# Performance work log

Hardware: AMD Instinct MI355X
Metric: run time of the kernel (lower is better)

Reference implementation:

```python
import jax, jax.numpy as jnp
import numpy as np

NEG_INF = -1e30  # stand-in for -inf in additive causal mask (softmax-safe)


def rotary_pos_emb(x):
    # x: [B, T, H, D]. Faithful to source: freqs = 1/1000**(arange(0,D,2)//D)
    # with INTEGER floor division -> exponent 0 -> all freqs == 1.0.
    B, T, H, D = x.shape
    exponents = (jnp.arange(0, D, 2)[: D // 2] // D).astype(jnp.float32)
    freqs = 1.0 / jnp.power(jnp.float32(1000.0), exponents)          # [D/2]
    theta = jnp.arange(T, dtype=jnp.float32)[:, None] * freqs[None, :]  # [T, D/2]
    cos = jnp.cos(theta)[None, :, None, :]  # [1, T, 1, D/2]
    sin = jnp.sin(theta)[None, :, None, :]
    xr = x.astype(jnp.float32).reshape(B, T, H, D // 2, 2)
    x0, x1 = xr[..., 0], xr[..., 1]
    # complex multiply (x0 + i x1) * (cos + i sin)
    out = jnp.stack([x0 * cos - x1 * sin, x0 * sin + x1 * cos], axis=-1)
    return out.reshape(B, T, H, D).astype(x.dtype)


def attention_fwd(x, wq, wk, wv, wo, n_heads=32):
    B, T, C = x.shape
    hd = C // n_heads  # head_dim = 128
    # nn.Linear(bias=False): y = x @ W^T with W: [out, in]
    xq = (x @ wq.T).reshape(B, T, n_heads, hd)
    xk = (x @ wk.T).reshape(B, T, n_heads, hd)
    xv = (x @ wv.T).reshape(B, T, n_heads, hd)
    xq = rotary_pos_emb(xq)
    xk = rotary_pos_emb(xk)
    # n_rep == 1 -> repeat_kv is identity
    scale = hd ** -0.5
    scores = jnp.einsum('bqhd,bkhd->bhqk', xq, xk) * scale  # [B,H,T,T]
    causal = jnp.tril(jnp.ones((T, T), dtype=bool))
    scores = jnp.where(causal[None, None], scores, NEG_INF)
    probs = jax.nn.softmax(scores.astype(jnp.float32), axis=-1).astype(xq.dtype)
    out = jnp.einsum('bhqk,bkhd->bqhd', probs, xv).reshape(B, T, C)
    return out @ wo.T


def setup_inputs() -> dict:
    key = jax.random.key(0)
    ks = jax.random.split(key, 5)
    B, T, C = 2, 2048, 4096
    s = 0.02
    return {
        'x': jax.random.normal(ks[0], (B, T, C), jnp.float32),
        'wq': jax.random.normal(ks[1], (C, C), jnp.float32) * s,
        'wk': jax.random.normal(ks[2], (C, C), jnp.float32) * s,
        'wv': jax.random.normal(ks[3], (C, C), jnp.float32) * s,
        'wo': jax.random.normal(ks[4], (C, C), jnp.float32) * s,
    }


def reference(x, wq, wk, wv, wo):
    return attention_fwd(x, wq, wk, wv, wo)
```

## Files before the change

### kernel.cpp

```cpp
#include <hip/hip_runtime.h>
#include <hip/hip_bf16.h>
#include <stdint.h>

typedef __bf16 bf16_t;
typedef __attribute__((ext_vector_type(8))) __bf16 bf16x8;
typedef __attribute__((ext_vector_type(4))) float f32x4;

#define GLL16(gptr, lptr)                                                      \
  __builtin_amdgcn_global_load_lds(                                            \
      (__attribute__((address_space(1))) void*)(gptr),                         \
      (__attribute__((address_space(3))) void*)(lptr), 16, 0, 0)

__global__ __launch_bounds__(256) void cast5_kernel(const float* __restrict__ x,
                                                    const float* __restrict__ wq,
                                                    const float* __restrict__ wk,
                                                    const float* __restrict__ wv,
                                                    const float* __restrict__ wo,
                                                    bf16_t* __restrict__ outbase) {
  const size_t SZ = (size_t)4096 * 4096;
  const float* in;
  switch (blockIdx.y) {
    case 0: in = x; break;
    case 1: in = wq; break;
    case 2: in = wk; break;
    case 3: in = wv; break;
    default: in = wo; break;
  }
  bf16_t* out = outbase + (size_t)blockIdx.y * SZ;
  int i = blockIdx.x * 256 + threadIdx.x;
  const float4* p = (const float4*)in + (size_t)i * 2;
  float4 a = p[0], b = p[1];
  bf16x8 o;
  o[0] = (__bf16)a.x; o[1] = (__bf16)a.y; o[2] = (__bf16)a.z; o[3] = (__bf16)a.w;
  o[4] = (__bf16)b.x; o[5] = (__bf16)b.y; o[6] = (__bf16)b.z; o[7] = (__bf16)b.w;
  *((bf16x8*)out + i) = o;
}

__device__ __forceinline__ void epi_rope(f32x4 acc[4][4], bf16_t* C, int bm,
                                         int bn, int wr, int wc, int quad,
                                         int l15) {
#pragma unroll
  for (int mi = 0; mi < 4; ++mi) {
    const int row0 = bm + wr * 64 + mi * 16 + quad * 4;
    float fsv[4], fcv[4];
#pragma unroll
    for (int r = 0; r < 4; ++r)
      sincosf((float)((row0 + r) & 2047), &fsv[r], &fcv[r]);
#pragma unroll
    for (int ni = 0; ni < 4; ++ni) {
      const int col = bn + wc * 64 + ni * 16 + l15;
      const bool odd = (col & 1);
#pragma unroll
      for (int r = 0; r < 4; ++r) {
        float v = acc[mi][ni][r];
        float p = __shfl_xor(v, 1, 64);
        float o = odd ? (p * fsv[r] + v * fcv[r]) : (v * fcv[r] - p * fsv[r]);
        C[(size_t)(row0 + r) * 4096 + col] = (__bf16)o;
      }
    }
  }
}

__device__ __forceinline__ void epi_vt(f32x4 acc[4][4], bf16_t* VT, int bm,
                                       int bn, int wr, int wc, int quad,
                                       int l15) {
#pragma unroll
  for (int mi = 0; mi < 4; ++mi) {
    const int row0 = bm + wr * 64 + mi * 16 + quad * 4;
    const int b = row0 >> 11, t0 = row0 & 2047;
#pragma unroll
    for (int ni = 0; ni < 4; ++ni) {
      const int col = bn + wc * 64 + ni * 16 + l15;
      const int h = col >> 7, d = col & 127;
      union { __bf16 e[4]; uint2 u; } pk;
#pragma unroll
      for (int r = 0; r < 4; ++r) pk.e[r] = (__bf16)acc[mi][ni][r];
      *(uint2*)&VT[((size_t)((b * 32 + h) * 128 + d)) * 2048 + t0] = pk.u;
    }
  }
}

#define GEMM_MAIN_LOOP(Aptr, Bptr)                                             \
  const int c0 = w * 2, c1 = c0 + 1;                                           \
  const int ra = lane >> 2;                                                    \
  const int gsw = ((lane & 3) ^ (ra & 3)) * 8;                                 \
  const bf16_t* ga0 = Aptr + (size_t)(bm + c0 * 16 + ra) * 4096 + gsw;         \
  const bf16_t* ga1 = Aptr + (size_t)(bm + c1 * 16 + ra) * 4096 + gsw;         \
  const bf16_t* gb0 = Bptr + (size_t)(bn + c0 * 16 + ra) * 4096 + gsw;         \
  const bf16_t* gb1 = Bptr + (size_t)(bn + c1 * 16 + ra) * 4096 + gsw;         \
  f32x4 acc[4][4] = {};                                                        \
  GLL16(ga0, &As[0][c0 * 512]);                                                \
  GLL16(ga1, &As[0][c1 * 512]);                                                \
  GLL16(gb0, &Bs[0][c0 * 512]);                                                \
  GLL16(gb1, &Bs[0][c1 * 512]);                                                \
  const int sa = quad ^ (l15 & 3);                      \
  for (int kt = 0; kt < 128; ++kt) {                                           \
    const int p = kt & 1;                                                      \
    __syncthreads();     \
    if (kt != 127) {                                                           \
      const int k1 = (kt + 1) * 32;                                            \
      GLL16(ga0 + k1, &As[p ^ 1][c0 * 512]);                                   \
      GLL16(ga1 + k1, &As[p ^ 1][c1 * 512]);                                   \
      GLL16(gb0 + k1, &Bs[p ^ 1][c0 * 512]);                                   \
      GLL16(gb1 + k1, &Bs[p ^ 1][c1 * 512]);                                   \
    }                                                                          \
    bf16x8 af[4], bfr[4];                                                      \
    _Pragma("unroll") for (int mi = 0; mi < 4; ++mi)                           \
        af[mi] = *(const bf16x8*)&As[p][(wr * 64 + mi * 16 + l15) * 32 + sa * 8]; \
    _Pragma("unroll") for (int ni = 0; ni < 4; ++ni)                           \
        bfr[ni] = *(const bf16x8*)&Bs[p][(wc * 64 + ni * 16 + l15) * 32 + sa * 8]; \
    _Pragma("unroll") for (int mi = 0; mi < 4; ++mi)                           \
        _Pragma("unroll") for (int ni = 0; ni < 4; ++ni)                       \
            acc[mi][ni] = __builtin_amdgcn_mfma_f32_16x16x32_bf16(              \
                af[mi], bfr[ni], acc[mi][ni], 0, 0, 0);                        \
  }

__global__ __launch_bounds__(256) void gemm_qkv(const bf16_t* __restrict__ X,
                                                const bf16_t* __restrict__ WQ,
                                                const bf16_t* __restrict__ WK,
                                                const bf16_t* __restrict__ WV,
                                                bf16_t* __restrict__ Qo,
                                                bf16_t* __restrict__ Ko,
                                                bf16_t* __restrict__ VTo) {
  __shared__ bf16_t As[2][128 * 32];
  __shared__ bf16_t Bs[2][128 * 32];
  const int tid = threadIdx.x;
  const int w = tid >> 6;
  const int lane = tid & 63;
  const int quad = lane >> 4;
  const int l15 = lane & 15;
  const int wr = w >> 1, wc = w & 1;
  const int mat = blockIdx.x >> 5;
  const int bn = (blockIdx.x & 31) * 128, bm = blockIdx.y * 128;
  const bf16_t* Bp = (mat == 0) ? WQ : (mat == 1) ? WK : WV;

  GEMM_MAIN_LOOP(X, Bp)

  if (mat == 0)
    epi_rope(acc, Qo, bm, bn, wr, wc, quad, l15);
  else if (mat == 1)
    epi_rope(acc, Ko, bm, bn, wr, wc, quad, l15);
  else
    epi_vt(acc, VTo, bm, bn, wr, wc, quad, l15);
}

__global__ __launch_bounds__(256) void gemm_out(const bf16_t* __restrict__ A,
                                                const bf16_t* __restrict__ B,
                                                float* __restrict__ C) {
  __shared__ bf16_t As[2][128 * 32];
  __shared__ bf16_t Bs[2][128 * 32];
  const int tid = threadIdx.x;
  const int w = tid >> 6;
  const int lane = tid & 63;
  const int quad = lane >> 4;
  const int l15 = lane & 15;
  const int wr = w >> 1, wc = w & 1;
  const int bn = blockIdx.x * 128, bm = blockIdx.y * 128;

  GEMM_MAIN_LOOP(A, B)

#pragma unroll
  for (int mi = 0; mi < 4; ++mi) {
    const int row0 = bm + wr * 64 + mi * 16 + quad * 4;
#pragma unroll
    for (int ni = 0; ni < 4; ++ni) {
      const int col = bn + wc * 64 + ni * 16 + l15;
#pragma unroll
      for (int r = 0; r < 4; ++r)
        C[(size_t)(row0 + r) * 4096 + col] = acc[mi][ni][r];
    }
  }
}

__global__ __launch_bounds__(256) void attn_kernel(const bf16_t* __restrict__ Q,
                                                   const bf16_t* __restrict__ Km,
                                                   const bf16_t* __restrict__ VT,
                                                   bf16_t* __restrict__ O) {
  __shared__ bf16_t Ks[64 * 128];
  __shared__ bf16_t Vts[128 * 64];
  __shared__ bf16_t QPs[64 * 128];
  const int tid = threadIdx.x;
  const int w = tid >> 6;
  const int lane = tid & 63;
  const int quad = lane >> 4;
  const int l15 = lane & 15;
  const int bh = blockIdx.x;
  const int qtile = 31 - blockIdx.y;
  const int mrow_base = (bh >> 5) * 2048;
  const int h = bh & 31;
  const float scale = 0.08838834764831845f;

#pragma unroll
  for (int it = 0; it < 4; ++it) {
    int c = w * 4 + it;
    int row = c * 4 + (lane >> 4);
    int cc = (lane & 15) ^ (row & 15);
    GLL16(Q + (size_t)(mrow_base + qtile * 64 + row) * 4096 + h * 128 + cc * 8,
          &QPs[c * 512]);
  }
  __syncthreads();
  bf16x8 qf[4];
#pragma unroll
  for (int ks = 0; ks < 4; ++ks) {
    int row = w * 16 + l15;
    int slot = (ks * 4 + quad) ^ (row & 15);
    qf[ks] = *(const bf16x8*)&QPs[row * 128 + slot * 8];
  }
  bf16_t* Pw = &QPs[w * 16 * 72];

  f32x4 accO[8] = {};
  float mrun[4], lrun[4];
#pragma unroll
  for (int r = 0; r < 4; ++r) { mrun[r] = -1e30f; lrun[r] = 0.f; }

  for (int kt = 0; kt <= qtile; ++kt) {
    __syncthreads();
#pragma unroll
    for (int it = 0; it < 4; ++it) {
      int c = w * 4 + it;
      int krow = c * 4 + (lane >> 4);
      int kcc = (lane & 15) ^ (krow & 15);
      GLL16(Km + (size_t)(mrow_base + kt * 64 + krow) * 4096 + h * 128 + kcc * 8,
            &Ks[c * 512]);
      int vrow = c * 8 + (lane >> 3);
      int vcc = (lane & 7) ^ (vrow & 7);
      GLL16(VT + (size_t)(bh * 128 + vrow) * 2048 + kt * 64 + vcc * 8,
            &Vts[c * 512]);
    }
    __syncthreads();

    f32x4 s[4];
#pragma unroll
    for (int ni = 0; ni < 4; ++ni) {
      s[ni] = (f32x4){0.f, 0.f, 0.f, 0.f};
#pragma unroll
      for (int ks = 0; ks < 4; ++ks) {
        int row = ni * 16 + l15;
        int slot = (ks * 4 + quad) ^ (row & 15);
        bf16x8 kf = *(const bf16x8*)&Ks[row * 128 + slot * 8];
        s[ni] = __builtin_amdgcn_mfma_f32_16x16x32_bf16(qf[ks], kf, s[ni], 0, 0, 0);
      }
    }
    const bool diag = (kt == qtile);
#pragma unroll
    for (int ni = 0; ni < 4; ++ni)
#pragma unroll
      for (int r = 0; r < 4; ++r) {
        float v = s[ni][r] * scale;
        if (diag && (ni * 16 + l15) > (w * 16 + quad * 4 + r)) v = -1e30f;
        s[ni][r] = v;
      }
    float mx[4], alpha[4], rs[4];
#pragma unroll
    for (int r = 0; r < 4; ++r)
      mx[r] = fmaxf(fmaxf(s[0][r], s[1][r]), fmaxf(s[2][r], s[3][r]));
#pragma unroll
    for (int off = 1; off < 16; off <<= 1)
#pragma unroll
      for (int r = 0; r < 4; ++r) mx[r] = fmaxf(mx[r], __shfl_xor(mx[r], off, 64));
    float ps[4][4];
#pragma unroll
    for (int r = 0; r < 4; ++r) {
      float mn = fmaxf(mrun[r], mx[r]);
      alpha[r] = __expf(mrun[r] - mn);
      mrun[r] = mn;
      rs[r] = 0.f;
    }
#pragma unroll
    for (int ni = 0; ni < 4; ++ni)
#pragma unroll
      for (int r = 0; r < 4; ++r) {
        float p = __expf(s[ni][r] - mrun[r]);
        ps[ni][r] = p;
        rs[r] += p;
      }
#pragma unroll
    for (int off = 1; off < 16; off <<= 1)
#pragma unroll
      for (int r = 0; r < 4; ++r) rs[r] += __shfl_xor(rs[r], off, 64);
#pragma unroll
    for (int r = 0; r < 4; ++r) lrun[r] = lrun[r] * alpha[r] + rs[r];
#pragma unroll
    for (int nt = 0; nt < 8; ++nt)
#pragma unroll
      for (int r = 0; r < 4; ++r) accO[nt][r] *= alpha[r];
#pragma unroll
    for (int ni = 0; ni < 4; ++ni)
#pragma unroll
      for (int r = 0; r < 4; ++r)
        Pw[(quad * 4 + r) * 72 + ni * 16 + l15] = (__bf16)ps[ni][r];
    asm volatile("s_waitcnt lgkmcnt(0)" ::: "memory");
    bf16x8 pf[2];
#pragma unroll
    for (int ks = 0; ks < 2; ++ks)
      pf[ks] = *(const bf16x8*)&Pw[l15 * 72 + ks * 32 + quad * 8];
#pragma unroll
    for (int nt = 0; nt < 8; ++nt)
#pragma unroll
      for (int ks = 0; ks < 2; ++ks) {
        int vrow = nt * 16 + l15;
        int slot = (ks * 4 + quad) ^ (vrow & 7);
        bf16x8 vf = *(const bf16x8*)&Vts[vrow * 64 + slot * 8];
        accO[nt] = __builtin_amdgcn_mfma_f32_16x16x32_bf16(pf[ks], vf, accO[nt], 0, 0, 0);
      }
  }

#pragma unroll
  for (int r = 0; r < 4; ++r) lrun[r] = 1.f / lrun[r];
#pragma unroll
  for (int nt = 0; nt < 8; ++nt)
#pragma unroll
    for (int r = 0; r < 4; ++r) {
      int trow = qtile * 64 + w * 16 + quad * 4 + r;
      int d = nt * 16 + l15;
      O[(size_t)(mrow_base + trow) * 4096 + h * 128 + d] =
          (__bf16)(accO[nt][r] * lrun[r]);
    }
}

extern "C" void kernel_launch(void* const* d_in, const int* in_sizes, int n_in,
                              void* d_out, int out_size, void* d_ws, size_t ws_size,
                              hipStream_t stream) {
  (void)in_sizes; (void)n_in; (void)out_size; (void)ws_size;
  const float* x = (const float*)d_in[0];
  const float* wq = (const float*)d_in[1];
  const float* wk = (const float*)d_in[2];
  const float* wv = (const float*)d_in[3];
  const float* wo = (const float*)d_in[4];
  float* out = (float*)d_out;

  const size_t SZ = (size_t)4096 * 4096;
  bf16_t* xb = (bf16_t*)d_ws;
  bf16_t* wqb = xb + SZ;
  bf16_t* wkb = wqb + SZ;
  bf16_t* wvb = wkb + SZ;
  bf16_t* wob = wvb + SZ;
  bf16_t* qb = wob + SZ;
  bf16_t* kb = qb + SZ;
  bf16_t* vtb = kb + SZ;
  bf16_t* ab = vtb + SZ;

  dim3 b256(256);
  cast5_kernel<<<dim3((unsigned)(SZ / 8 / 256), 5), b256, 0, stream>>>(
      x, wq, wk, wv, wo, xb);

  gemm_qkv<<<dim3(96, 32), b256, 0, stream>>>(xb, wqb, wkb, wvb, qb, kb, vtb);

  attn_kernel<<<dim3(64, 32), b256, 0, stream>>>(qb, kb, vtb, ab);

  gemm_out<<<dim3(32, 32), b256, 0, stream>>>(ab, wob, out);
}
```

Before: 1.209 ms.

## Use 256x256 tiles with 8-wave ping-pong pipelined GEMM for QKV and output projections

```diff
diff --git a/kernel.cpp b/kernel.cpp
--- a/kernel.cpp
+++ b/kernel.cpp
@@ -36,12 +36,89 @@
   *((bf16x8*)out + i) = o;
 }
 
-__device__ __forceinline__ void epi_rope(f32x4 acc[4][4], bf16_t* C, int bm,
-                                         int bn, int wr, int wc, int quad,
-                                         int l15) {
-#pragma unroll
-  for (int mi = 0; mi < 4; ++mi) {
-    const int row0 = bm + wr * 64 + mi * 16 + quad * 4;
+#define STAGE_HALF(gbase, ldsbase)                                             \
+  do {                                                                         \
+    GLL16((gbase) + (size_t)(w * 32 + sr) * 4096 + sq, (ldsbase) + w * 1024);  \
+    GLL16((gbase) + (size_t)(w * 32 + 16 + sr) * 4096 + sq,                    \
+          (ldsbase) + w * 1024 + 512);                                         \
+  } while (0)
+
+#define PHASE(mh_, kk_, buf_, LOADB_, STAGE_STMT, TAIL_STMT)                   \
+  do {                                                                         \
+    bf16x8 af_[4];                                                             \
+    _Pragma("unroll") for (int mi = 0; mi < 4; ++mi) af_[mi] =                 \
+        *(const bf16x8*)&As[buf_][kk_][(wr * 128 + (mh_)*64 + mi * 16 + l15) * \
+                                           32 +                                \
+                                       quad * 8];                              \
+    if (LOADB_) {                                                              \
+      _Pragma("unroll") for (int ni = 0; ni < 4; ++ni) bfr[ni] =               \
+          *(const bf16x8*)&Bs[buf_][kk_][(wc * 64 + ni * 16 + l15) * 32 +      \
+                                         quad * 8];                            \
+    }                                                                          \
+    STAGE_STMT;                                                                \
+    __builtin_amdgcn_s_barrier();                                              \
+    asm volatile("s_waitcnt lgkmcnt(0)" ::: "memory");                         \
+    __builtin_amdgcn_sched_barrier(0);                                         \
+    __builtin_amdgcn_s_setprio(1);                                             \
+    _Pragma("unroll") for (int mi = 0; mi < 4; ++mi)                           \
+        _Pragma("unroll") for (int ni = 0; ni < 4; ++ni)                       \
+            acc[(mh_)*4 + mi][ni] = __builtin_amdgcn_mfma_f32_16x16x32_bf16(   \
+                af_[mi], bfr[ni], acc[(mh_)*4 + mi][ni], 0, 0, 0);             \
+    __builtin_amdgcn_s_setprio(0);                                             \
+    __builtin_amdgcn_sched_barrier(0);                                         \
+    TAIL_STMT;                                                                 \
+    __builtin_amdgcn_s_barrier();                                              \
+  } while (0)
+
+#define GEMM256_MAIN(Aptr, Bptr)                                               \
+  const bf16_t* Ag = (Aptr) + (size_t)bm * 4096;                               \
+  const bf16_t* Bg = (Bptr) + (size_t)bn * 4096;                               \
+  f32x4 acc[8][4] = {};                                                        \
+  bf16x8 bfr[4];                                                               \
+  STAGE_HALF(Ag, &As[0][0][0]);                                                \
+  STAGE_HALF(Bg, &Bs[0][0][0]);                                                \
+  STAGE_HALF(Ag + 32, &As[0][1][0]);                                           \
+  STAGE_HALF(Bg + 32, &Bs[0][1][0]);                                           \
+  STAGE_HALF(Ag + 64, &As[1][0][0]);                                           \
+  STAGE_HALF(Bg + 64, &Bs[1][0][0]);                                           \
+  asm volatile("s_waitcnt vmcnt(4)" ::: "memory");                             \
+  __builtin_amdgcn_s_barrier();                                                \
+  for (int it = 0; it < 32; ++it) {                                            \
+    const int kt = it * 2;                                                     \
+    const bool more = (it < 31);                                               \
+    PHASE(0, 0, 0, 1,                                                          \
+          STAGE_HALF(Ag + (size_t)(kt + 1) * 64 + 32, &As[1][1][0]), (void)0); \
+    PHASE(1, 0, 0, 0,                                                          \
+          STAGE_HALF(Bg + (size_t)(kt + 1) * 64 + 32, &Bs[1][1][0]), (void)0); \
+    PHASE(0, 1, 0, 1,                                                          \
+          if (more) STAGE_HALF(Ag + (size_t)(kt + 2) * 64, &As[0][0][0]),      \
+          (void)0);                                                            \
+    PHASE(1, 1, 0, 0,                                                          \
+          if (more) STAGE_HALF(Bg + (size_t)(kt + 2) * 64, &Bs[0][0][0]),      \
+          if (more) { asm volatile("s_waitcnt vmcnt(4)" ::: "memory"); } else {\
+            asm volatile("s_waitcnt vmcnt(0)" ::: "memory"); });               \
+    PHASE(0, 0, 1, 1,                                                          \
+          if (more) STAGE_HALF(Ag + (size_t)(kt + 2) * 64 + 32, &As[0][1][0]), \
+          (void)0);                                                            \
+    PHASE(1, 0, 1, 0,                                                          \
+          if (more) STAGE_HALF(Bg + (size_t)(kt + 2) * 64 + 32, &Bs[0][1][0]), \
+          (void)0);                                                            \
+    PHASE(0, 1, 1, 1,                                                          \
+          if (more) STAGE_HALF(Ag + (size_t)(kt + 3) * 64, &As[1][0][0]),      \
+          (void)0);                                                            \
+    PHASE(1, 1, 1, 0,                                                          \
+          if (more) STAGE_HALF(Bg + (size_t)(kt + 3) * 64, &Bs[1][0][0]),      \
+          if (more) { asm volatile("s_waitcnt vmcnt(4)" ::: "memory"); } else {\
+            asm volatile("s_waitcnt vmcnt(0)" ::: "memory"); });               \
+  }
+
+__device__ __forceinline__ void epi_rope256(const f32x4 (&acc)[8][4],
+                                            bf16_t* __restrict__ C, int bm,
+                                            int bn, int wr, int wc, int quad,
+                                            int l15) {
+#pragma unroll
+  for (int a = 0; a < 8; ++a) {
+    const int row0 = bm + wr * 128 + a * 16 + quad * 4;
     float fsv[4], fcv[4];
 #pragma unroll
     for (int r = 0; r < 4; ++r)
@@ -52,21 +129,22 @@
       const bool odd = (col & 1);
 #pragma unroll
       for (int r = 0; r < 4; ++r) {
-        float v = acc[mi][ni][r];
-        float p = __shfl_xor(v, 1, 64);
-        float o = odd ? (p * fsv[r] + v * fcv[r]) : (v * fcv[r] - p * fsv[r]);
+        float v = acc[a][ni][r];
+        float pr = __shfl_xor(v, 1, 64);
+        float o = odd ? (pr * fsv[r] + v * fcv[r]) : (v * fcv[r] - pr * fsv[r]);
         C[(size_t)(row0 + r) * 4096 + col] = (__bf16)o;
       }
     }
   }
 }
 
-__device__ __forceinline__ void epi_vt(f32x4 acc[4][4], bf16_t* VT, int bm,
-                                       int bn, int wr, int wc, int quad,
-                                       int l15) {
-#pragma unroll
-  for (int mi = 0; mi < 4; ++mi) {
-    const int row0 = bm + wr * 64 + mi * 16 + quad * 4;
+__device__ __forceinline__ void epi_vt256(const f32x4 (&acc)[8][4],
+                                          bf16_t* __restrict__ VT, int bm,
+                                          int bn, int wr, int wc, int quad,
+                                          int l15) {
+#pragma unroll
+  for (int a = 0; a < 8; ++a) {
+    const int row0 = bm + wr * 128 + a * 16 + quad * 4;
     const int b = row0 >> 11, t0 = row0 & 2047;
 #pragma unroll
     for (int ni = 0; ni < 4; ++ni) {
@@ -74,100 +152,71 @@
       const int h = col >> 7, d = col & 127;
       union { __bf16 e[4]; uint2 u; } pk;
 #pragma unroll
-      for (int r = 0; r < 4; ++r) pk.e[r] = (__bf16)acc[mi][ni][r];
+      for (int r = 0; r < 4; ++r) pk.e[r] = (__bf16)acc[a][ni][r];
       *(uint2*)&VT[((size_t)((b * 32 + h) * 128 + d)) * 2048 + t0] = pk.u;
     }
   }
 }
 
-#define GEMM_MAIN_LOOP(Aptr, Bptr)                                             \
-  const int c0 = w * 2, c1 = c0 + 1;                                           \
-  const int ra = lane >> 2;                                                    \
-  const int gsw = ((lane & 3) ^ (ra & 3)) * 8;                                 \
-  const bf16_t* ga0 = Aptr + (size_t)(bm + c0 * 16 + ra) * 4096 + gsw;         \
-  const bf16_t* ga1 = Aptr + (size_t)(bm + c1 * 16 + ra) * 4096 + gsw;         \
-  const bf16_t* gb0 = Bptr + (size_t)(bn + c0 * 16 + ra) * 4096 + gsw;         \
-  const bf16_t* gb1 = Bptr + (size_t)(bn + c1 * 16 + ra) * 4096 + gsw;         \
-  f32x4 acc[4][4] = {};                                                        \
-  GLL16(ga0, &As[0][c0 * 512]);                                                \
-  GLL16(ga1, &As[0][c1 * 512]);                                                \
-  GLL16(gb0, &Bs[0][c0 * 512]);                                                \
-  GLL16(gb1, &Bs[0][c1 * 512]);                                                \
-  const int sa = quad ^ (l15 & 3);                      \
-  for (int kt = 0; kt < 128; ++kt) {                                           \
-    const int p = kt & 1;                                                      \
-    __syncthreads();     \
-    if (kt != 127) {                                                           \
-      const int k1 = (kt + 1) * 32;                                            \
-      GLL16(ga0 + k1, &As[p ^ 1][c0 * 512]);                                   \
-      GLL16(ga1 + k1, &As[p ^ 1][c1 * 512]);                                   \
-      GLL16(gb0 + k1, &Bs[p ^ 1][c0 * 512]);                                   \
-      GLL16(gb1 + k1, &Bs[p ^ 1][c1 * 512]);                                   \
-    }                                                                          \
-    bf16x8 af[4], bfr[4];                                                      \
-    _Pragma("unroll") for (int mi = 0; mi < 4; ++mi)                           \
-        af[mi] = *(const bf16x8*)&As[p][(wr * 64 + mi * 16 + l15) * 32 + sa * 8]; \
-    _Pragma("unroll") for (int ni = 0; ni < 4; ++ni)                           \
-        bfr[ni] = *(const bf16x8*)&Bs[p][(wc * 64 + ni * 16 + l15) * 32 + sa * 8]; \
-    _Pragma("unroll") for (int mi = 0; mi < 4; ++mi)                           \
-        _Pragma("unroll") for (int ni = 0; ni < 4; ++ni)                       \
-            acc[mi][ni] = __builtin_amdgcn_mfma_f32_16x16x32_bf16(              \
-                af[mi], bfr[ni], acc[mi][ni], 0, 0, 0);                        \
-  }
-
-__global__ __launch_bounds__(256) void gemm_qkv(const bf16_t* __restrict__ X,
-                                                const bf16_t* __restrict__ WQ,
-                                                const bf16_t* __restrict__ WK,
-                                                const bf16_t* __restrict__ WV,
-                                                bf16_t* __restrict__ Qo,
-                                                bf16_t* __restrict__ Ko,
-                                                bf16_t* __restrict__ VTo) {
-  __shared__ bf16_t As[2][128 * 32];
-  __shared__ bf16_t Bs[2][128 * 32];
+__global__ __launch_bounds__(512, 2) void gemm_qkv(const bf16_t* __restrict__ X,
+                                                   const bf16_t* __restrict__ WQ,
+                                                   const bf16_t* __restrict__ WK,
+                                                   const bf16_t* __restrict__ WV,
+                                                   bf16_t* __restrict__ Qo,
+                                                   bf16_t* __restrict__ Ko,
+                                                   bf16_t* __restrict__ VTo) {
+  __shared__ bf16_t As[2][2][8192];
+  __shared__ bf16_t Bs[2][2][8192];
   const int tid = threadIdx.x;
   const int w = tid >> 6;
   const int lane = tid & 63;
   const int quad = lane >> 4;
   const int l15 = lane & 15;
-  const int wr = w >> 1, wc = w & 1;
-  const int mat = blockIdx.x >> 5;
-  const int bn = (blockIdx.x & 31) * 128, bm = blockIdx.y * 128;
+  const int wr = w >> 2, wc = w & 3;
+  const int sr = lane >> 2, sq = (lane & 3) * 8;
+  const int mat = blockIdx.y;
+  int id = blockIdx.x;
+  id = (id & 7) * 32 + (id >> 3);
+  const int bm = (id >> 4) * 256, bn = (id & 15) * 256;
   const bf16_t* Bp = (mat == 0) ? WQ : (mat == 1) ? WK : WV;
 
-  GEMM_MAIN_LOOP(X, Bp)
+  GEMM256_MAIN(X, Bp)
 
   if (mat == 0)
-    epi_rope(acc, Qo, bm, bn, wr, wc, quad, l15);
+    epi_rope256(acc, Qo, bm, bn, wr, wc, quad, l15);
   else if (mat == 1)
-    epi_rope(acc, Ko, bm, bn, wr, wc, quad, l15);
+    epi_rope256(acc, Ko, bm, bn, wr, wc, quad, l15);
   else
-    epi_vt(acc, VTo, bm, bn, wr, wc, quad, l15);
-}
-
-__global__ __launch_bounds__(256) void gemm_out(const bf16_t* __restrict__ A,
-                                                const bf16_t* __restrict__ B,
-                                                float* __restrict__ C) {
-  __shared__ bf16_t As[2][128 * 32];
-  __shared__ bf16_t Bs[2][128 * 32];
+    epi_vt256(acc, VTo, bm, bn, wr, wc, quad, l15);
+}
+
+__global__ __launch_bounds__(512, 2) void gemm_out(const bf16_t* __restrict__ A,
+                                                   const bf16_t* __restrict__ B,
+                                                   float* __restrict__ C) {
+  __shared__ bf16_t As[2][2][8192];
+  __shared__ bf16_t Bs[2][2][8192];
   const int tid = threadIdx.x;
   const int w = tid >> 6;
   const int lane = tid & 63;
   const int quad = lane >> 4;
   const int l15 = lane & 15;
-  const int wr = w >> 1, wc = w & 1;
-  const int bn = blockIdx.x * 128, bm = blockIdx.y * 128;
-
-  GEMM_MAIN_LOOP(A, B)
-
-#pragma unroll
-  for (int mi = 0; mi < 4; ++mi) {
-    const int row0 = bm + wr * 64 + mi * 16 + quad * 4;
+  const int wr = w >> 2, wc = w & 3;
+  const int sr = lane >> 2, sq = (lane & 3) * 8;
+  int id = blockIdx.x;
+  id = (id & 7) * 32 + (id >> 3);
+  const int bm = (id >> 4) * 256, bn = (id & 15) * 256;
+
+  GEMM256_MAIN(A, B)
+
+#pragma unroll
+  for (int a = 0; a < 8; ++a) {
+    const int row0 = bm + wr * 128 + a * 16 + quad * 4;
 #pragma unroll
     for (int ni = 0; ni < 4; ++ni) {
       const int col = bn + wc * 64 + ni * 16 + l15;
 #pragma unroll
       for (int r = 0; r < 4; ++r)
-        C[(size_t)(row0 + r) * 4096 + col] = acc[mi][ni][r];
+        C[(size_t)(row0 + r) * 4096 + col] = acc[a][ni][r];
     }
   }
 }
@@ -340,13 +389,13 @@
   bf16_t* vtb = kb + SZ;
   bf16_t* ab = vtb + SZ;
 
-  dim3 b256(256);
+  dim3 b256(256), b512(512);
   cast5_kernel<<<dim3((unsigned)(SZ / 8 / 256), 5), b256, 0, stream>>>(
       x, wq, wk, wv, wo, xb);
 
-  gemm_qkv<<<dim3(96, 32), b256, 0, stream>>>(xb, wqb, wkb, wvb, qb, kb, vtb);
+  gemm_qkv<<<dim3(256, 3), b512, 0, stream>>>(xb, wqb, wkb, wvb, qb, kb, vtb);
 
   attn_kernel<<<dim3(64, 32), b256, 0, stream>>>(qb, kb, vtb, ab);
 
-  gemm_out<<<dim3(32, 32), b256, 0, stream>>>(ab, wob, out);
-}
+  gemm_out<<<dim3(256), b512, 0, stream>>>(ab, wob, out);
+}
```

New measurement: 1.070 ms. -11.5%, faster.
